# Optimization experiments

Measured on AMD Instinct MI355X. Metric: run time of the kernel, lower is better.

The kernel has to match this reference:

```python
import jax, jax.numpy as jnp
import numpy as np

# graph sizes
G, P, EP = 128, 256, 1024          # graphs, nodes/graph, edges/graph
N, E = G * P, G * EP
C, KENS, S = 4, 2, 1               # centroids, ensembles, samples
R = S * KENS                       # repeats
F, DE, D, OUT = 64, 16, 128, 10


def setup_inputs() -> dict:
    key = jax.random.key(0)
    ks = jax.random.split(key, 24)
    off = (jnp.arange(G, dtype=jnp.int32) * P)[:, None]
    src = (jax.random.randint(ks[0], (G, EP), 0, P, dtype=jnp.int32) + off).reshape(-1)
    dst = (jax.random.randint(ks[1], (G, EP), 0, P, dtype=jnp.int32) + off).reshape(-1)
    edge_index = jnp.stack([src, dst])            # [2, E], edges stay within graphs
    batch = jnp.repeat(jnp.arange(G, dtype=jnp.int32), P)  # [N]
    rn = lambda k, shp, s: jax.random.normal(k, shp, jnp.float32) * s
    return {
        "x_feat": rn(ks[2], (N, F), 1.0),
        "edge_attr": rn(ks[3], (E, DE), 1.0),
        "W_atom": rn(ks[4], (F, D), 0.1), "b_atom": jnp.zeros((D,), jnp.float32),
        "W_score": rn(ks[5], (D, C * KENS), 0.1),
        "W_edge": rn(ks[6], (DE, D), 0.1),
        "W_b2c": rn(ks[7], (D, D), 0.1),
        "W_bb": rn(ks[8], (D, D), 0.1), "W_bc": rn(ks[9], (D, D), 0.1),
        "W_cb": rn(ks[10], (D, D), 0.1), "W_cc": rn(ks[11], (D, D), 0.1),
        "W_sb": rn(ks[12], (D, D), 0.1), "W_sc": rn(ks[13], (D, D), 0.1),
        "W_inter": rn(ks[14], (D, D), 0.1), "b_inter": jnp.zeros((D,), jnp.float32),
        "W_out": rn(ks[15], (D, OUT), 0.1), "b_out": jnp.zeros((OUT,), jnp.float32),
        "edge_index": edge_index, "batch": batch,
    }


def reference(x_feat, edge_attr, W_atom, b_atom, W_score, W_edge, W_b2c,
              W_bb, W_bc, W_cb, W_cc, W_sb, W_sc, W_inter, b_inter,
              W_out, b_out, edge_index, batch):
    src, dst = edge_index[0], edge_index[1]
    # atom encoder + scorer + softmax sampler (marginals)
    x = x_feat @ W_atom + b_atom                                  # [N,D]
    scores = (x @ W_score).reshape(N, C, KENS)
    marg = jax.nn.softmax(scores, axis=1)                         # over centroids
    nm = jnp.broadcast_to(marg[None], (S, N, C, KENS))            # [S,N,C,KENS]
    nm = jnp.transpose(nm, (0, 3, 2, 1)).reshape(R, C, N)         # [R,C,N]
    em = nm[:, :, src] * nm[:, :, dst]                            # edge_mask [R,C,E]
    # base2centroid: masked MP on base graph + weighted segment-mean pooling
    edge_emb = edge_attr @ W_edge                                 # [E,D]
    h = jax.nn.relu(x @ W_b2c)                                    # [N,D]
    m = h[src] + edge_emb                                         # [E,D]
    agg = jnp.zeros((R, C, N, D), m.dtype).at[:, :, dst].add(em[..., None] * m)
    hm = h[None, None] + agg                                      # [R,C,N,D]
    denom = jnp.zeros((R, C, G), nm.dtype).at[:, :, batch].add(nm)
    num = jnp.zeros((R, C, G, D), hm.dtype).at[:, :, batch].add(nm[..., None] * hm)
    cent_x = jnp.transpose(num / (denom[..., None] + 1e-6), (0, 2, 1, 3))  # [R,G,C,D]
    # intra centroid-pair edge weights: triu pairs + diag, scatter over graphs
    iu, ju = np.triu_indices(C, 1)
    pi = np.concatenate([iu, np.arange(C)])
    pj = np.concatenate([ju, np.arange(C)])
    e2g = batch[src]
    w = jnp.zeros((R, pi.size, G), nm.dtype).at[:, :, e2g].add(
        nm[:, pi][:, :, src] * nm[:, pj][:, :, dst])              # [R,10,G]
    w = w.at[:, -C:, :].multiply(0.5)                             # halve diagonal counts
    wt = jnp.transpose(w, (0, 2, 1))                              # [R,G,10]
    Wcc = jnp.zeros((R, G, C, C), nm.dtype)
    Wcc = Wcc.at[:, :, pi, pj].add(wt).at[:, :, pj, pi].add(wt)   # to_undirected
    dg = jnp.arange(C)
    Wcc = Wcc.at[:, :, dg, dg].multiply(0.5)                      # self loops counted once
    Wcc = Wcc / (jax.lax.stop_gradient(jnp.max(Wcc)) + 1e-9)      # detached-max norm
    # hetero GNN layer: base->base, base->centroid, centroid->centroid, centroid->base
    agg_bb = jnp.zeros((N, D), x.dtype).at[dst].add(x[src] + edge_emb)           # [N,D]
    agg_bc = jnp.transpose(
        jnp.zeros((R, C, G, D), x.dtype).at[:, :, batch].add(nm[..., None] * x[None, None]),
        (0, 2, 1, 3))                                             # [R,G,C,D]
    agg_cc = jnp.einsum('rgij,rgjd->rgid', Wcc, cent_x)
    h_cent = jax.nn.relu(agg_bc @ W_bc + agg_cc @ W_cc + cent_x @ W_sc)          # [R,G,C,D]
    agg_cb = jnp.einsum('rcn,rncd->rnd', nm, h_cent[:, batch])                   # [R,N,D]
    h_base = jax.nn.relu(agg_bb[None] @ W_bb + agg_cb @ W_cb + x[None] @ W_sb)   # [R,N,D]
    # inter-ensemble mean pool, inter head, intra mean graph pool, intra head
    node_emb = jnp.mean(h_base, axis=0) @ W_inter + b_inter                      # [N,D]
    graph_emb = jnp.zeros((G, D), node_emb.dtype).at[batch].add(node_emb) / P    # [G,D]
    return graph_emb @ W_out + b_out                                             # [G,OUT]
```

## Files before the change

kernel.cpp:

```cpp
#include <hip/hip_runtime.h>
#include <hip/hip_bf16.h>

#define Nn 32768
#define Ee 131072
#define Gg 128
#define Dd 128

using bf16 = __hip_bfloat16;
typedef __attribute__((ext_vector_type(8))) short bf16x8;
typedef __attribute__((ext_vector_type(4))) float f32x4;

__device__ __forceinline__ float b2f(bf16 v){ return __bfloat162float(v); }
__device__ __forceinline__ bf16  f2b(float v){ return __float2bfloat16(v); }
__device__ __forceinline__ unsigned short bf16bits(float v){
  union { bf16 b; unsigned short u; } cv; cv.b = f2b(v); return cv.u;
}
__device__ __forceinline__ float bfu(unsigned short u){
  return __uint_as_float((unsigned int)u << 16);
}
__device__ __forceinline__ float upk_x(unsigned int v){ return __uint_as_float(v << 16); }
__device__ __forceinline__ float upk_h(unsigned int v){ return __uint_as_float(v & 0xffff0000u); }

__global__ __launch_bounds__(128)
void k_wrep(const float* __restrict__ Wbb, const float* __restrict__ Wsb,
            const float* __restrict__ Wcb, const float* __restrict__ Wa,
            const float* __restrict__ Wb2c,
            unsigned short* __restrict__ Wbbp, unsigned short* __restrict__ Wsbp,
            unsigned short* __restrict__ Wcbp, unsigned short* __restrict__ Wap,
            unsigned short* __restrict__ Wb2cp) {
  int mat = blockIdx.x >> 7, n = blockIdx.x & 127, k = threadIdx.x;
  if      (mat == 0) Wbbp [n*128 + k] = bf16bits(Wbb [k*128 + n]);
  else if (mat == 1) Wsbp [n*128 + k] = bf16bits(Wsb [k*128 + n]);
  else if (mat == 2) Wcbp [n*128 + k] = bf16bits(Wcb [k*128 + n]);
  else if (mat == 3) { if (k < 64) Wap[n*64 + k] = bf16bits(Wa[k*128 + n]); }
  else               Wb2cp[n*128 + k] = bf16bits(Wb2c[k*128 + n]);
}

__global__ __launch_bounds__(256)
void k_atom(const float* __restrict__ xf, const unsigned short* __restrict__ Wap,
            const float* __restrict__ ba, const float* __restrict__ Wsc,
            const unsigned short* __restrict__ Wb2cp,
            unsigned int* __restrict__ xh, float* __restrict__ nmt) {
  __shared__ unsigned short sxf[64*72];
  __shared__ unsigned short sxb[64*136];
  __shared__ float ss[64*8];
  __shared__ float sWsc[1024];
  int tid = threadIdx.x, n0 = blockIdx.x*64;
  int lane = tid & 63, wv = tid >> 6;
  int m = lane & 15, quad = lane >> 4;
  int rbase = wv*16;
  #pragma unroll
  for (int k = 0; k < 4; ++k) {
    int pos = (tid + k*256)*4;
    int node = pos >> 6, f = pos & 63;
    float4 v = *reinterpret_cast<const float4*>(xf + (size_t)n0*64 + pos);
    ushort4 o;
    o.x = bf16bits(v.x); o.y = bf16bits(v.y); o.z = bf16bits(v.z); o.w = bf16bits(v.w);
    *reinterpret_cast<ushort4*>(&sxf[node*72 + f]) = o;
  }
  for (int j = tid; j < 1024; j += 256) sWsc[j] = Wsc[j];
  __syncthreads();
  f32x4 cx[8];
  #pragma unroll
  for (int nt = 0; nt < 8; ++nt) {
    float bv = ba[nt*16 + m];
    cx[nt] = (f32x4){bv, bv, bv, bv};
  }
  const unsigned short* a1 = &sxf[(rbase + m)*72];
  #pragma unroll
  for (int nt = 0; nt < 8; ++nt) {
    #pragma unroll
    for (int kk = 0; kk < 2; ++kk) {
      int ko = kk*32 + quad*8;
      bf16x8 av = *reinterpret_cast<const bf16x8*>((const short*)a1 + ko);
      bf16x8 bv8 = *reinterpret_cast<const bf16x8*>((const short*)Wap + (nt*16 + m)*64 + ko);
      cx[nt] = __builtin_amdgcn_mfma_f32_16x16x32_bf16(av, bv8, cx[nt], 0, 0, 0);
    }
  }
  #pragma unroll
  for (int nt = 0; nt < 8; ++nt)
    #pragma unroll
    for (int i = 0; i < 4; ++i)
      sxb[(rbase + quad*4 + i)*136 + nt*16 + m] = bf16bits(cx[nt][i]);
  __syncthreads();
  for (int p = tid; p < 512; p += 256) {
    int node = p >> 3, col = p & 7;
    float s = 0.f;
    for (int dd = 0; dd < 128; ++dd)
      s += bfu(sxb[node*136 + dd]) * sWsc[dd*8 + col];
    ss[node*8 + col] = s;
  }
  __syncthreads();
  if (tid < 128) {
    int node = tid >> 1, k = tid & 1;
    float v0 = ss[node*8 + 0 + k], v1 = ss[node*8 + 2 + k];
    float v2 = ss[node*8 + 4 + k], v3 = ss[node*8 + 6 + k];
    float mx = fmaxf(fmaxf(v0, v1), fmaxf(v2, v3));
    float e0 = expf(v0-mx), e1 = expf(v1-mx), e2 = expf(v2-mx), e3 = expf(v3-mx);
    float inv = 1.f / (e0+e1+e2+e3);
    *reinterpret_cast<float4*>(nmt + (size_t)(n0 + node)*8 + k*4) =
        make_float4(e0*inv, e1*inv, e2*inv, e3*inv);
  }
  f32x4 chf[8];
  #pragma unroll
  for (int nt = 0; nt < 8; ++nt) chf[nt] = (f32x4){0.f,0.f,0.f,0.f};
  const unsigned short* a2 = &sxb[(rbase + m)*136];
  #pragma unroll
  for (int nt = 0; nt < 8; ++nt) {
    #pragma unroll
    for (int kk = 0; kk < 4; ++kk) {
      int ko = kk*32 + quad*8;
      bf16x8 av = *reinterpret_cast<const bf16x8*>((const short*)a2 + ko);
      bf16x8 bv8 = *reinterpret_cast<const bf16x8*>((const short*)Wb2cp + (nt*16 + m)*128 + ko);
      chf[nt] = __builtin_amdgcn_mfma_f32_16x16x32_bf16(av, bv8, chf[nt], 0, 0, 0);
    }
  }
  #pragma unroll
  for (int nt = 0; nt < 8; ++nt) {
    #pragma unroll
    for (int i = 0; i < 4; ++i) {
      int row = rbase + quad*4 + i, col = nt*16 + m;
      float hv = fmaxf(chf[nt][i], 0.f);
      unsigned short xb = sxb[row*136 + col];
      xh[(size_t)(n0 + row)*128 + col] =
          ((unsigned int)bf16bits(hv) << 16) | (unsigned int)xb;
    }
  }
}

__global__ __launch_bounds__(256)
void k_csr(const int* __restrict__ ei, const float* __restrict__ nmt,
           int* __restrict__ osrc, int* __restrict__ oeid,
           int* __restrict__ rowstart, float* __restrict__ den) {
  __shared__ int cnt[256], off[256], sdl[1024], ssl[1024];
  __shared__ float den8[8];
  int t = threadIdx.x, g = blockIdx.x;
  cnt[t] = 0;
  if (t < 8) den8[t] = 0.f;
  __syncthreads();
  #pragma unroll
  for (int j = 0; j < 4; ++j) {
    int e = t + j*256;
    int sl = ei[g*1024 + e] - g*256;
    int dl = ei[Ee + g*1024 + e] - g*256;
    ssl[e] = sl; sdl[e] = dl;
    atomicAdd(&cnt[dl], 1);
  }
  {
    const float4* p = reinterpret_cast<const float4*>(nmt + (size_t)(g*256 + t)*8);
    float4 a = p[0], b = p[1];
    float v[8] = {a.x,a.y,a.z,a.w,b.x,b.y,b.z,b.w};
    #pragma unroll
    for (int i = 0; i < 8; ++i) {
      float s = v[i];
      for (int o = 32; o > 0; o >>= 1) s += __shfl_xor(s, o);
      if ((t & 63) == 0) atomicAdd(&den8[i], s);
    }
  }
  __syncthreads();
  off[t] = cnt[t];
  __syncthreads();
  for (int s = 1; s < 256; s <<= 1) {
    int v = (t >= s) ? off[t - s] : 0;
    __syncthreads();
    off[t] += v;
    __syncthreads();
  }
  int startv = off[t] - cnt[t];
  rowstart[g*256 + t] = startv;
  off[t] = startv;
  __syncthreads();
  #pragma unroll
  for (int j = 0; j < 4; ++j) {
    int e = t + j*256;
    int pos = atomicAdd(&off[sdl[e]], 1);
    osrc[g*1024 + pos] = g*256 + ssl[e];
    oeid[g*1024 + pos] = e;
  }
  if (t < 8) den[t*Gg + g] = den8[t];
}

__global__ __launch_bounds__(256)
void k_edge(const int* __restrict__ ei, const float* __restrict__ nmt,
            const float* __restrict__ ea, float* __restrict__ bnmp,
            float* __restrict__ geap, float* __restrict__ wsump) {
  __shared__ float eaT[16*260];
  __shared__ float salT[8*260];
  __shared__ float sbeta[8*260];
  __shared__ float red[20];
  __shared__ float sga[256];
  int t = threadIdx.x, bq = blockIdx.x;
  int g = bq >> 2;
  int ebase = g*1024 + (bq & 3)*256;
  for (int j = t; j < 2080; j += 256) sbeta[j] = 0.f;
  if (t < 20) red[t] = 0.f;
  __syncthreads();
  int sl = ei[ebase + t] - g*256;
  int dl = ei[Ee + ebase + t] - g*256;
  const float4* ps4 = reinterpret_cast<const float4*>(nmt + (size_t)(g*256 + sl)*8);
  const float4* pt4 = reinterpret_cast<const float4*>(nmt + (size_t)(g*256 + dl)*8);
  float4 sv0 = ps4[0], sv1 = ps4[1], tv0 = pt4[0], tv1 = pt4[1];
  float ps[8] = {sv0.x,sv0.y,sv0.z,sv0.w,sv1.x,sv1.y,sv1.z,sv1.w};
  float pt[8] = {tv0.x,tv0.y,tv0.z,tv0.w,tv1.x,tv1.y,tv1.z,tv1.w};
  float w20[20];
  #pragma unroll
  for (int r = 0; r < 2; ++r) {
    int b = r*4;
    w20[r*10+0] = ps[b+0]*pt[b+1]; w20[r*10+1] = ps[b+0]*pt[b+2];
    w20[r*10+2] = ps[b+0]*pt[b+3]; w20[r*10+3] = ps[b+1]*pt[b+2];
    w20[r*10+4] = ps[b+1]*pt[b+3]; w20[r*10+5] = ps[b+2]*pt[b+3];
    w20[r*10+6] = ps[b+0]*pt[b+0]; w20[r*10+7] = ps[b+1]*pt[b+1];
    w20[r*10+8] = ps[b+2]*pt[b+2]; w20[r*10+9] = ps[b+3]*pt[b+3];
  }
  #pragma unroll
  for (int rc = 0; rc < 8; ++rc) {
    float al = ps[rc]*pt[rc]*pt[rc];
    salT[rc*260 + t] = al;
    atomicAdd(&sbeta[rc*260 + sl], al);
  }
  {
    const float4* ea4 = reinterpret_cast<const float4*>(ea + (size_t)ebase*16);
    #pragma unroll
    for (int k = 0; k < 4; ++k) {
      float4 v = ea4[t*4 + k];
      eaT[(k*4+0)*260 + t] = v.x;
      eaT[(k*4+1)*260 + t] = v.y;
      eaT[(k*4+2)*260 + t] = v.z;
      eaT[(k*4+3)*260 + t] = v.w;
    }
  }
  #pragma unroll
  for (int i = 0; i < 20; ++i) {
    for (int o = 32; o > 0; o >>= 1) w20[i] += __shfl_down(w20[i], o);
  }
  if ((t & 63) == 0) {
    #pragma unroll
    for (int i = 0; i < 20; ++i) atomicAdd(&red[i], w20[i]);
  }
  __syncthreads();
  {
    int rc = t >> 5, j = (t >> 1) & 15, hf = t & 1;
    float a = 0.f;
    int eb = hf*128;
    for (int ee = eb; ee < eb + 128; ++ee)
      a += salT[rc*260 + ee] * eaT[j*260 + ee];
    sga[t] = a;
  }
  __syncthreads();
  if ((t & 1) == 0) {
    int rc = t >> 5, j = (t >> 1) & 15;
    geap[(size_t)bq*128 + rc*16 + j] = sga[t] + sga[t+1];
  }
  if (t < 20) wsump[bq*20 + t] = red[t];
  {
    float4* bo = reinterpret_cast<float4*>(bnmp + (size_t)bq*2048 + t*8);
    bo[0] = make_float4(sbeta[0*260+t], sbeta[1*260+t], sbeta[2*260+t], sbeta[3*260+t]);
    bo[1] = make_float4(sbeta[4*260+t], sbeta[5*260+t], sbeta[6*260+t], sbeta[7*260+t]);
  }
}

__global__ __launch_bounds__(256)
void k_sea(const float* __restrict__ ea, const int* __restrict__ oeid,
           const int* __restrict__ rowstart, float* __restrict__ sea) {
  int t = threadIdx.x;
  int n = blockIdx.x*16 + (t >> 4);
  int j = t & 15;
  int g = n >> 8;
  int start = rowstart[n];
  int end = ((n & 255) == 255) ? 1024 : rowstart[n+1];
  float s = 0.f;
  for (int jj = start; jj < end; ++jj) {
    int e = oeid[g*1024 + jj];
    s += ea[((size_t)g*1024 + e)*16 + j];
  }
  sea[(size_t)n*16 + j] = s;
}

__global__ __launch_bounds__(128)
void k_wfin(const float* __restrict__ wsump, float* __restrict__ wcc,
            float* __restrict__ maxv) {
  __shared__ float smax[128];
  int t = threadIdx.x;
  float w[20];
  #pragma unroll
  for (int i = 0; i < 20; ++i)
    w[i] = wsump[(t*4+0)*20 + i] + wsump[(t*4+1)*20 + i]
         + wsump[(t*4+2)*20 + i] + wsump[(t*4+3)*20 + i];
  float mx = 0.f;
  #pragma unroll
  for (int r = 0; r < 2; ++r) {
    #pragma unroll
    for (int ij = 0; ij < 16; ++ij) {
      int i = ij >> 2, j = ij & 3;
      float v;
      if (i == j) v = 0.5f * w[r*10 + 6 + i];
      else { int a = i < j ? i : j, b = i < j ? j : i;
             int p = (a == 0) ? (b - 1) : (a == 1) ? (b + 1) : 5;
             v = w[r*10 + p]; }
      wcc[(r*Gg + t)*16 + ij] = v;
      mx = fmaxf(mx, v);
    }
  }
  smax[t] = mx;
  __syncthreads();
  for (int s = 64; s > 0; s >>= 1) {
    if (t < s) smax[t] = fmaxf(smax[t], smax[t + s]);
    __syncthreads();
  }
  if (t == 0) maxv[0] = smax[0];
}

__global__ __launch_bounds__(256)
void k_pool(const unsigned int* __restrict__ xh, const float* __restrict__ nmt,
            const float* __restrict__ bnmp, float* __restrict__ pnum,
            float* __restrict__ pabc) {
  __shared__ float combN[8*128], combA[8*128];
  int t = threadIdx.x, d = t & 127, q = t >> 7;
  int g = blockIdx.x >> 4, e16 = blockIdx.x & 15;
  int nbase = g*256 + e16*16;
  float aH[8] = {0,0,0,0,0,0,0,0};
  float aX[8] = {0,0,0,0,0,0,0,0};
  for (int nn = q; nn < 16; nn += 2) {
    int n = nbase + nn;
    int ln = n & 255;
    unsigned int vn = xh[(size_t)n*128 + d];
    float xn = upk_x(vn), hn = upk_h(vn);
    const float4* pp = reinterpret_cast<const float4*>(nmt + (size_t)n*8);
    float4 p0 = pp[0], p1 = pp[1];
    float pc[8] = {p0.x,p0.y,p0.z,p0.w,p1.x,p1.y,p1.z,p1.w};
    float bt[8] = {0,0,0,0,0,0,0,0};
    #pragma unroll
    for (int qq = 0; qq < 4; ++qq) {
      const float4* bp = reinterpret_cast<const float4*>(bnmp + (size_t)(g*4+qq)*2048 + ln*8);
      float4 b0 = bp[0], b1 = bp[1];
      bt[0]+=b0.x; bt[1]+=b0.y; bt[2]+=b0.z; bt[3]+=b0.w;
      bt[4]+=b1.x; bt[5]+=b1.y; bt[6]+=b1.z; bt[7]+=b1.w;
    }
    #pragma unroll
    for (int rc = 0; rc < 8; ++rc) {
      aH[rc] += (pc[rc] + bt[rc])*hn;
      aX[rc] += pc[rc]*xn;
    }
  }
  if (q == 1) {
    #pragma unroll
    for (int rc = 0; rc < 8; ++rc) { combN[rc*128+d] = aH[rc]; combA[rc*128+d] = aX[rc]; }
  }
  __syncthreads();
  if (q == 0) {
    #pragma unroll
    for (int rc = 0; rc < 8; ++rc) {
      pnum[(((size_t)rc*Gg + g)*16 + e16)*128 + d] = aH[rc] + combN[rc*128+d];
      pabc[(((size_t)rc*Gg + g)*16 + e16)*128 + d] = aX[rc] + combA[rc*128+d];
    }
  }
}

__global__ __launch_bounds__(256)
void k_aggx(const unsigned int* __restrict__ xh, const float* __restrict__ sea,
            const float* __restrict__ We, const int* __restrict__ osrc,
            const int* __restrict__ rowstart, unsigned short* __restrict__ aggbb16) {
  int t = threadIdx.x, d = t & 127, q = t >> 7;
  int g = blockIdx.x >> 5, e32 = blockIdx.x & 31;
  int nbase = g*256 + e32*8;
  float w[16];
  #pragma unroll
  for (int j = 0; j < 16; ++j) w[j] = We[j*128 + d];
  for (int nn = q; nn < 8; nn += 2) {
    int n = nbase + nn;
    const float4* sp = reinterpret_cast<const float4*>(sea + (size_t)n*16);
    float4 s0 = sp[0], s1 = sp[1], s2 = sp[2], s3 = sp[3];
    float agg = s0.x*w[0] + s0.y*w[1] + s0.z*w[2] + s0.w*w[3]
              + s1.x*w[4] + s1.y*w[5] + s1.z*w[6] + s1.w*w[7]
              + s2.x*w[8] + s2.y*w[9] + s2.z*w[10]+ s2.w*w[11]
              + s3.x*w[12]+ s3.y*w[13]+ s3.z*w[14]+ s3.w*w[15];
    int ln = n & 255;
    int start = rowstart[n];
    int end = (ln == 255) ? 1024 : rowstart[n+1];
    for (int jj = start; jj < end; ++jj) {
      int sg = osrc[g*1024 + jj];
      agg += upk_x(xh[(size_t)sg*128 + d]);
    }
    aggbb16[(size_t)n*128 + d] = bf16bits(agg);
  }
}

__global__ __launch_bounds__(128)
void k_hcent(const float* __restrict__ pnum, const float* __restrict__ den,
             const float* __restrict__ pabc, const float* __restrict__ geap,
             const float* __restrict__ We, const float* __restrict__ wcc,
             const float* __restrict__ maxv,
             const float* __restrict__ Wbc, const float* __restrict__ Wcc_,
             const float* __restrict__ Wsc2, float* __restrict__ hcent) {
  __shared__ float scent[512], sbc[512], sccs[512], swcc[16], sgea[64];
  int tid = threadIdx.x, r = blockIdx.x >> 7, g = blockIdx.x & 127;
  float inv = 1.f / (maxv[0] + 1e-9f);
  if (tid < 16) swcc[tid] = wcc[(r*Gg + g)*16 + tid] * inv;
  if (tid < 64) {
    int c = tid >> 4, j = tid & 15;
    int idx = (r*4 + c)*16 + j;
    sgea[tid] = geap[(size_t)(g*4+0)*128 + idx] + geap[(size_t)(g*4+1)*128 + idx]
              + geap[(size_t)(g*4+2)*128 + idx] + geap[(size_t)(g*4+3)*128 + idx];
  }
  __syncthreads();
  for (int c = 0; c < 4; ++c) {
    int rc = r*4 + c;
    float nv = 0.f, av = 0.f;
    #pragma unroll
    for (int s = 0; s < 16; ++s) {
      nv += pnum[(((size_t)rc*Gg + g)*16 + s)*128 + tid];
      av += pabc[(((size_t)rc*Gg + g)*16 + s)*128 + tid];
    }
    #pragma unroll
    for (int j = 0; j < 16; ++j) nv += sgea[c*16 + j] * We[j*128 + tid];
    float dn = den[rc*Gg + g] + 1e-6f;
    scent[c*128 + tid] = nv / dn;
    sbc[c*128 + tid]   = av;
  }
  __syncthreads();
  for (int i = 0; i < 4; ++i) {
    sccs[i*128 + tid] = swcc[i*4+0]*scent[tid]       + swcc[i*4+1]*scent[128 + tid]
                      + swcc[i*4+2]*scent[256 + tid] + swcc[i*4+3]*scent[384 + tid];
  }
  __syncthreads();
  float acc[4] = {0.f, 0.f, 0.f, 0.f};
  for (int k = 0; k < 128; ++k) {
    float wb = Wbc[k*128 + tid], wc = Wcc_[k*128 + tid], ws2 = Wsc2[k*128 + tid];
    #pragma unroll
    for (int c = 0; c < 4; ++c)
      acc[c] += sbc[c*128 + k]*wb + sccs[c*128 + k]*wc + scent[c*128 + k]*ws2;
  }
  #pragma unroll
  for (int c = 0; c < 4; ++c)
    hcent[((r*Gg + g)*4 + c)*128 + tid] = fmaxf(acc[c], 0.f);
}

__global__ __launch_bounds__(256)
void k_hbase(const unsigned short* __restrict__ aggbb16,
             const unsigned int* __restrict__ xh,
             const float* __restrict__ nmt, const float* __restrict__ hcent,
             const unsigned short* __restrict__ Wbbp,
             const unsigned short* __restrict__ Wsbp,
             const unsigned short* __restrict__ Wcbp,
             float* __restrict__ pgsum) {
  __shared__ unsigned short A1[64*136];
  __shared__ unsigned short A2[64*136];
  __shared__ float shc[512];
  __shared__ float snm[256];
  __shared__ float pred[128];
  int tid = threadIdx.x, n0 = blockIdx.x*64, g = n0 >> 8;
  int lane = tid & 63, wv = tid >> 6;
  int m = lane & 15, quad = lane >> 4;
  int rbase = wv*16;
  for (int j = tid; j < 1024; j += 256) {
    int row = j >> 4, col = (j & 15) * 8;
    uint4 v = *reinterpret_cast<const uint4*>(aggbb16 + (size_t)(n0+row)*128 + col);
    *reinterpret_cast<uint4*>(&A1[row*136 + col]) = v;
  }
  for (int j = tid; j < 2048; j += 256) {
    int row = j >> 5, col = (j & 31) * 4;
    uint4 v = *reinterpret_cast<const uint4*>(xh + (size_t)(n0+row)*128 + col);
    uint2 o;
    o.x = (v.x & 0xffffu) | (v.y << 16);
    o.y = (v.z & 0xffffu) | (v.w << 16);
    *reinterpret_cast<uint2*>(&A2[row*136 + col]) = o;
  }
  __syncthreads();
  f32x4 bb[8];
  #pragma unroll
  for (int nt = 0; nt < 8; ++nt) bb[nt] = (f32x4){0.f,0.f,0.f,0.f};
  const short* a1r = (const short*)&A1[(rbase + m)*136];
  const short* a2r = (const short*)&A2[(rbase + m)*136];
  #pragma unroll
  for (int nt = 0; nt < 8; ++nt) {
    #pragma unroll
    for (int kk = 0; kk < 4; ++kk) {
      int ko = kk*32 + quad*8;
      bf16x8 av1 = *reinterpret_cast<const bf16x8*>(a1r + ko);
      bf16x8 wv1 = *reinterpret_cast<const bf16x8*>((const short*)Wbbp + (nt*16 + m)*128 + ko);
      bb[nt] = __builtin_amdgcn_mfma_f32_16x16x32_bf16(av1, wv1, bb[nt], 0, 0, 0);
      bf16x8 av2 = *reinterpret_cast<const bf16x8*>(a2r + ko);
      bf16x8 wv2 = *reinterpret_cast<const bf16x8*>((const short*)Wsbp + (nt*16 + m)*128 + ko);
      bb[nt] = __builtin_amdgcn_mfma_f32_16x16x32_bf16(av2, wv2, bb[nt], 0, 0, 0);
    }
  }
  __syncthreads();
  unsigned short* SB = A2;
  f32x4 msum[8];
  #pragma unroll
  for (int nt = 0; nt < 8; ++nt) msum[nt] = (f32x4){0.f,0.f,0.f,0.f};
  for (int r = 0; r < 2; ++r) {
    for (int j = tid; j < 512; j += 256) shc[j] = hcent[((size_t)(r*Gg + g)*4)*128 + j];
    if (tid < 256) snm[tid] = nmt[(size_t)(n0 + (tid >> 2))*8 + r*4 + (tid & 3)];
    __syncthreads();
    for (int j = tid; j < 8192; j += 256) {
      int node = j >> 7, k = j & 127;
      float v = snm[node*4+0]*shc[k]       + snm[node*4+1]*shc[128 + k]
              + snm[node*4+2]*shc[256 + k] + snm[node*4+3]*shc[384 + k];
      SB[node*136 + k] = bf16bits(v);
    }
    __syncthreads();
    f32x4 aw[8];
    #pragma unroll
    for (int nt = 0; nt < 8; ++nt) aw[nt] = (f32x4){0.f,0.f,0.f,0.f};
    const short* sbr = (const short*)&SB[(rbase + m)*136];
    #pragma unroll
    for (int nt = 0; nt < 8; ++nt) {
      #pragma unroll
      for (int kk = 0; kk < 4; ++kk) {
        int ko = kk*32 + quad*8;
        bf16x8 av = *reinterpret_cast<const bf16x8*>(sbr + ko);
        bf16x8 wvv = *reinterpret_cast<const bf16x8*>((const short*)Wcbp + (nt*16 + m)*128 + ko);
        aw[nt] = __builtin_amdgcn_mfma_f32_16x16x32_bf16(av, wvv, aw[nt], 0, 0, 0);
      }
    }
    #pragma unroll
    for (int nt = 0; nt < 8; ++nt) {
      #pragma unroll
      for (int i = 0; i < 4; ++i)
        msum[nt][i] += 0.5f * fmaxf(bb[nt][i] + aw[nt][i], 0.f);
    }
    __syncthreads();
  }
  if (tid < 128) pred[tid] = 0.f;
  __syncthreads();
  #pragma unroll
  for (int nt = 0; nt < 8; ++nt) {
    float s = msum[nt][0] + msum[nt][1] + msum[nt][2] + msum[nt][3];
    atomicAdd(&pred[nt*16 + m], s);
  }
  __syncthreads();
  if (tid < 128) pgsum[(size_t)blockIdx.x*128 + tid] = pred[tid];
}

__global__ __launch_bounds__(128)
void k_out(const float* __restrict__ pgsum, const float* __restrict__ Wint,
           const float* __restrict__ bint, const float* __restrict__ Wout,
           const float* __restrict__ bout, float* __restrict__ out) {
  __shared__ float ss[128], sge[128];
  int tid = threadIdx.x, g = blockIdx.x;
  float s = pgsum[(size_t)(g*4+0)*128 + tid] + pgsum[(size_t)(g*4+1)*128 + tid]
          + pgsum[(size_t)(g*4+2)*128 + tid] + pgsum[(size_t)(g*4+3)*128 + tid];
  ss[tid] = s * (1.f/256.f);
  __syncthreads();
  float ge = bint[tid];
  for (int k = 0; k < 128; ++k) ge += ss[k] * Wint[k*128 + tid];
  sge[tid] = ge;
  __syncthreads();
  if (tid < 10) {
    float o = bout[tid];
    for (int d = 0; d < 128; ++d) o += sge[d] * Wout[d*10 + tid];
    out[g*10 + tid] = o;
  }
}

extern "C" void kernel_launch(void* const* d_in, const int* in_sizes, int n_in,
                              void* d_out, int out_size, void* d_ws, size_t ws_size,
                              hipStream_t stream) {
  const float* xf   = (const float*)d_in[0];
  const float* ea   = (const float*)d_in[1];
  const float* Wa   = (const float*)d_in[2];
  const float* ba   = (const float*)d_in[3];
  const float* Wsc  = (const float*)d_in[4];
  const float* We   = (const float*)d_in[5];
  const float* Wb2c = (const float*)d_in[6];
  const float* Wbb  = (const float*)d_in[7];
  const float* Wbc  = (const float*)d_in[8];
  const float* Wcb  = (const float*)d_in[9];
  const float* WccW = (const float*)d_in[10];
  const float* Wsb  = (const float*)d_in[11];
  const float* Wsc2 = (const float*)d_in[12];
  const float* Wint = (const float*)d_in[13];
  const float* bint = (const float*)d_in[14];
  const float* Wout = (const float*)d_in[15];
  const float* bout = (const float*)d_in[16];
  const int*   ei   = (const int*)d_in[17];

  float* ws    = (float*)d_ws;
  unsigned int* xh = (unsigned int*)ws;
  float* nmt   = ws + 4194304;
  float* hcent = ws + 4456448;
  float* wcc   = ws + 4587520;
  unsigned short* aggbb16 = (unsigned short*)(ws + 4591616);
  int*   osrc  = (int*)(ws + 6688768);
  int*   oeid  = (int*)(ws + 6819840);
  int*   rowst = (int*)(ws + 6950912);
  float* sea   = ws + 6983680;
  float* bnmp  = ws + 7507968;
  float* geap  = ws + 8556544;
  float* wsump = ws + 8622080;
  float* pnum  = ws + 8632320;
  float* pabc  = ws + 10729472;
  float* den   = ws + 12826624;
  float* pgsum = ws + 12827648;
  float* maxv  = ws + 12893184;
  unsigned short* Wbbp  = (unsigned short*)(ws + 12893248);
  unsigned short* Wsbp  = (unsigned short*)(ws + 12901440);
  unsigned short* Wcbp  = (unsigned short*)(ws + 12909632);
  unsigned short* Wap   = (unsigned short*)(ws + 12917824);
  unsigned short* Wb2cp = (unsigned short*)(ws + 12921920);

  k_wrep <<<5*128, 128, 0, stream>>>(Wbb, Wsb, Wcb, Wa, Wb2c,
                                     Wbbp, Wsbp, Wcbp, Wap, Wb2cp);
  k_atom <<<Nn/64, 256, 0, stream>>>(xf, Wap, ba, Wsc, Wb2cp, xh, nmt);
  k_csr  <<<Gg,    256, 0, stream>>>(ei, nmt, osrc, oeid, rowst, den);
  k_edge <<<Gg*4,  256, 0, stream>>>(ei, nmt, ea, bnmp, geap, wsump);
  k_sea  <<<Nn/16, 256, 0, stream>>>(ea, oeid, rowst, sea);
  k_wfin <<<1,     128, 0, stream>>>(wsump, wcc, maxv);
  k_pool <<<Gg*16, 256, 0, stream>>>(xh, nmt, bnmp, pnum, pabc);
  k_aggx <<<Gg*32, 256, 0, stream>>>(xh, sea, We, osrc, rowst, aggbb16);
  k_hcent<<<2*Gg,  128, 0, stream>>>(pnum, den, pabc, geap, We, wcc, maxv,
                                     Wbc, WccW, Wsc2, hcent);
  k_hbase<<<Nn/64, 256, 0, stream>>>(aggbb16, xh, nmt, hcent, Wbbp, Wsbp, Wcbp, pgsum);
  k_out  <<<Gg,    128, 0, stream>>>(pgsum, Wint, bint, Wout, bout, (float*)d_out);
}
```

Baseline: 281.2 us.

## Merge CSR, edge, and sea kernels; fuse pool with base aggregation

```diff
diff --git a/kernel.cpp b/kernel.cpp
--- a/kernel.cpp
+++ b/kernel.cpp
@@ -129,151 +129,158 @@
 }
 
 __global__ __launch_bounds__(256)
-void k_csr(const int* __restrict__ ei, const float* __restrict__ nmt,
-           int* __restrict__ osrc, int* __restrict__ oeid,
-           int* __restrict__ rowstart, float* __restrict__ den) {
-  __shared__ int cnt[256], off[256], sdl[1024], ssl[1024];
-  __shared__ float den8[8];
-  int t = threadIdx.x, g = blockIdx.x;
-  cnt[t] = 0;
-  if (t < 8) den8[t] = 0.f;
-  __syncthreads();
-  #pragma unroll
-  for (int j = 0; j < 4; ++j) {
-    int e = t + j*256;
-    int sl = ei[g*1024 + e] - g*256;
-    int dl = ei[Ee + g*1024 + e] - g*256;
-    ssl[e] = sl; sdl[e] = dl;
-    atomicAdd(&cnt[dl], 1);
-  }
-  {
-    const float4* p = reinterpret_cast<const float4*>(nmt + (size_t)(g*256 + t)*8);
-    float4 a = p[0], b = p[1];
-    float v[8] = {a.x,a.y,a.z,a.w,b.x,b.y,b.z,b.w};
-    #pragma unroll
-    for (int i = 0; i < 8; ++i) {
-      float s = v[i];
-      for (int o = 32; o > 0; o >>= 1) s += __shfl_xor(s, o);
-      if ((t & 63) == 0) atomicAdd(&den8[i], s);
-    }
-  }
-  __syncthreads();
-  off[t] = cnt[t];
-  __syncthreads();
-  for (int s = 1; s < 256; s <<= 1) {
-    int v = (t >= s) ? off[t - s] : 0;
-    __syncthreads();
-    off[t] += v;
-    __syncthreads();
-  }
-  int startv = off[t] - cnt[t];
-  rowstart[g*256 + t] = startv;
-  off[t] = startv;
-  __syncthreads();
-  #pragma unroll
-  for (int j = 0; j < 4; ++j) {
-    int e = t + j*256;
-    int pos = atomicAdd(&off[sdl[e]], 1);
-    osrc[g*1024 + pos] = g*256 + ssl[e];
-    oeid[g*1024 + pos] = e;
-  }
-  if (t < 8) den[t*Gg + g] = den8[t];
-}
-
-__global__ __launch_bounds__(256)
-void k_edge(const int* __restrict__ ei, const float* __restrict__ nmt,
-            const float* __restrict__ ea, float* __restrict__ bnmp,
-            float* __restrict__ geap, float* __restrict__ wsump) {
-  __shared__ float eaT[16*260];
-  __shared__ float salT[8*260];
-  __shared__ float sbeta[8*260];
-  __shared__ float red[20];
-  __shared__ float sga[256];
-  int t = threadIdx.x, bq = blockIdx.x;
-  int g = bq >> 2;
-  int ebase = g*1024 + (bq & 3)*256;
-  for (int j = t; j < 2080; j += 256) sbeta[j] = 0.f;
-  if (t < 20) red[t] = 0.f;
-  __syncthreads();
-  int sl = ei[ebase + t] - g*256;
-  int dl = ei[Ee + ebase + t] - g*256;
-  const float4* ps4 = reinterpret_cast<const float4*>(nmt + (size_t)(g*256 + sl)*8);
-  const float4* pt4 = reinterpret_cast<const float4*>(nmt + (size_t)(g*256 + dl)*8);
-  float4 sv0 = ps4[0], sv1 = ps4[1], tv0 = pt4[0], tv1 = pt4[1];
-  float ps[8] = {sv0.x,sv0.y,sv0.z,sv0.w,sv1.x,sv1.y,sv1.z,sv1.w};
-  float pt[8] = {tv0.x,tv0.y,tv0.z,tv0.w,tv1.x,tv1.y,tv1.z,tv1.w};
-  float w20[20];
-  #pragma unroll
-  for (int r = 0; r < 2; ++r) {
-    int b = r*4;
-    w20[r*10+0] = ps[b+0]*pt[b+1]; w20[r*10+1] = ps[b+0]*pt[b+2];
-    w20[r*10+2] = ps[b+0]*pt[b+3]; w20[r*10+3] = ps[b+1]*pt[b+2];
-    w20[r*10+4] = ps[b+1]*pt[b+3]; w20[r*10+5] = ps[b+2]*pt[b+3];
-    w20[r*10+6] = ps[b+0]*pt[b+0]; w20[r*10+7] = ps[b+1]*pt[b+1];
-    w20[r*10+8] = ps[b+2]*pt[b+2]; w20[r*10+9] = ps[b+3]*pt[b+3];
-  }
-  #pragma unroll
-  for (int rc = 0; rc < 8; ++rc) {
-    float al = ps[rc]*pt[rc]*pt[rc];
-    salT[rc*260 + t] = al;
-    atomicAdd(&sbeta[rc*260 + sl], al);
-  }
-  {
-    const float4* ea4 = reinterpret_cast<const float4*>(ea + (size_t)ebase*16);
-    #pragma unroll
-    for (int k = 0; k < 4; ++k) {
-      float4 v = ea4[t*4 + k];
-      eaT[(k*4+0)*260 + t] = v.x;
-      eaT[(k*4+1)*260 + t] = v.y;
-      eaT[(k*4+2)*260 + t] = v.z;
-      eaT[(k*4+3)*260 + t] = v.w;
-    }
-  }
-  #pragma unroll
-  for (int i = 0; i < 20; ++i) {
-    for (int o = 32; o > 0; o >>= 1) w20[i] += __shfl_down(w20[i], o);
-  }
-  if ((t & 63) == 0) {
-    #pragma unroll
-    for (int i = 0; i < 20; ++i) atomicAdd(&red[i], w20[i]);
-  }
-  __syncthreads();
-  {
-    int rc = t >> 5, j = (t >> 1) & 15, hf = t & 1;
-    float a = 0.f;
-    int eb = hf*128;
-    for (int ee = eb; ee < eb + 128; ++ee)
-      a += salT[rc*260 + ee] * eaT[j*260 + ee];
-    sga[t] = a;
-  }
-  __syncthreads();
-  if ((t & 1) == 0) {
-    int rc = t >> 5, j = (t >> 1) & 15;
-    geap[(size_t)bq*128 + rc*16 + j] = sga[t] + sga[t+1];
-  }
-  if (t < 20) wsump[bq*20 + t] = red[t];
-  {
-    float4* bo = reinterpret_cast<float4*>(bnmp + (size_t)bq*2048 + t*8);
-    bo[0] = make_float4(sbeta[0*260+t], sbeta[1*260+t], sbeta[2*260+t], sbeta[3*260+t]);
-    bo[1] = make_float4(sbeta[4*260+t], sbeta[5*260+t], sbeta[6*260+t], sbeta[7*260+t]);
-  }
-}
-
-__global__ __launch_bounds__(256)
-void k_sea(const float* __restrict__ ea, const int* __restrict__ oeid,
-           const int* __restrict__ rowstart, float* __restrict__ sea) {
+void k_gedge(const int* __restrict__ ei, const float* __restrict__ nmt,
+             const float* __restrict__ ea,
+             int* __restrict__ osrc, int* __restrict__ rowstart,
+             float* __restrict__ sea, float* __restrict__ den,
+             float* __restrict__ bnmp, float* __restrict__ geap,
+             float* __restrict__ wsump) {
+  __shared__ __align__(16) char smem[34384];
   int t = threadIdx.x;
-  int n = blockIdx.x*16 + (t >> 4);
-  int j = t & 15;
-  int g = n >> 8;
-  int start = rowstart[n];
-  int end = ((n & 255) == 255) ? 1024 : rowstart[n+1];
-  float s = 0.f;
-  for (int jj = start; jj < end; ++jj) {
-    int e = oeid[g*1024 + jj];
-    s += ea[((size_t)g*1024 + e)*16 + j];
-  }
-  sea[(size_t)n*16 + j] = s;
+  if (blockIdx.x < Gg) {
+    int g = blockIdx.x;
+    int* cnt    = (int*)smem;
+    int* off    = cnt + 256;
+    int* sdl    = off + 256;
+    int* ssl    = sdl + 1024;
+    int* sorder = ssl + 1024;
+    float* den8 = (float*)(sorder + 1024);
+    cnt[t] = 0;
+    if (t < 8) den8[t] = 0.f;
+    __syncthreads();
+    #pragma unroll
+    for (int j = 0; j < 4; ++j) {
+      int e = t + j*256;
+      int sl = ei[g*1024 + e] - g*256;
+      int dl = ei[Ee + g*1024 + e] - g*256;
+      ssl[e] = sl; sdl[e] = dl;
+      atomicAdd(&cnt[dl], 1);
+    }
+    {
+      const float4* p = reinterpret_cast<const float4*>(nmt + (size_t)(g*256 + t)*8);
+      float4 a = p[0], b = p[1];
+      float v[8] = {a.x,a.y,a.z,a.w,b.x,b.y,b.z,b.w};
+      #pragma unroll
+      for (int i = 0; i < 8; ++i) {
+        float s = v[i];
+        for (int o = 32; o > 0; o >>= 1) s += __shfl_xor(s, o);
+        if ((t & 63) == 0) atomicAdd(&den8[i], s);
+      }
+    }
+    __syncthreads();
+    off[t] = cnt[t];
+    __syncthreads();
+    for (int s = 1; s < 256; s <<= 1) {
+      int v = (t >= s) ? off[t - s] : 0;
+      __syncthreads();
+      off[t] += v;
+      __syncthreads();
+    }
+    int startv = off[t] - cnt[t];
+    int mycnt = cnt[t];
+    rowstart[g*256 + t] = startv;
+    off[t] = startv;
+    __syncthreads();
+    #pragma unroll
+    for (int j = 0; j < 4; ++j) {
+      int e = t + j*256;
+      int pos = atomicAdd(&off[sdl[e]], 1);
+      osrc[g*1024 + pos] = g*256 + ssl[e];
+      sorder[pos] = e;
+    }
+    __syncthreads();
+    float s0x=0,s0y=0,s0z=0,s0w=0, s1x=0,s1y=0,s1z=0,s1w=0;
+    float s2x=0,s2y=0,s2z=0,s2w=0, s3x=0,s3y=0,s3z=0,s3w=0;
+    for (int jj = startv; jj < startv + mycnt; ++jj) {
+      int e = sorder[jj];
+      const float4* er = reinterpret_cast<const float4*>(ea + ((size_t)g*1024 + e)*16);
+      float4 a0 = er[0], a1 = er[1], a2 = er[2], a3 = er[3];
+      s0x+=a0.x; s0y+=a0.y; s0z+=a0.z; s0w+=a0.w;
+      s1x+=a1.x; s1y+=a1.y; s1z+=a1.z; s1w+=a1.w;
+      s2x+=a2.x; s2y+=a2.y; s2z+=a2.z; s2w+=a2.w;
+      s3x+=a3.x; s3y+=a3.y; s3z+=a3.z; s3w+=a3.w;
+    }
+    float4* so = reinterpret_cast<float4*>(sea + (size_t)(g*256 + t)*16);
+    so[0] = make_float4(s0x,s0y,s0z,s0w);
+    so[1] = make_float4(s1x,s1y,s1z,s1w);
+    so[2] = make_float4(s2x,s2y,s2z,s2w);
+    so[3] = make_float4(s3x,s3y,s3z,s3w);
+    if (t < 8) den[t*Gg + g] = den8[t];
+  } else {
+    int bq = blockIdx.x - Gg;
+    float* eaT   = (float*)smem;
+    float* salT  = eaT + 16*260;
+    float* sbeta = salT + 8*260;
+    float* red   = sbeta + 8*260;
+    float* sga   = red + 20;
+    int g = bq >> 2;
+    int ebase = g*1024 + (bq & 3)*256;
+    for (int j = t; j < 2080; j += 256) sbeta[j] = 0.f;
+    if (t < 20) red[t] = 0.f;
+    __syncthreads();
+    int sl = ei[ebase + t] - g*256;
+    int dl = ei[Ee + ebase + t] - g*256;
+    const float4* ps4 = reinterpret_cast<const float4*>(nmt + (size_t)(g*256 + sl)*8);
+    const float4* pt4 = reinterpret_cast<const float4*>(nmt + (size_t)(g*256 + dl)*8);
+    float4 sv0 = ps4[0], sv1 = ps4[1], tv0 = pt4[0], tv1 = pt4[1];
+    float ps[8] = {sv0.x,sv0.y,sv0.z,sv0.w,sv1.x,sv1.y,sv1.z,sv1.w};
+    float pt[8] = {tv0.x,tv0.y,tv0.z,tv0.w,tv1.x,tv1.y,tv1.z,tv1.w};
+    float w20[20];
+    #pragma unroll
+    for (int r = 0; r < 2; ++r) {
+      int b = r*4;
+      w20[r*10+0] = ps[b+0]*pt[b+1]; w20[r*10+1] = ps[b+0]*pt[b+2];
+      w20[r*10+2] = ps[b+0]*pt[b+3]; w20[r*10+3] = ps[b+1]*pt[b+2];
+      w20[r*10+4] = ps[b+1]*pt[b+3]; w20[r*10+5] = ps[b+2]*pt[b+3];
+      w20[r*10+6] = ps[b+0]*pt[b+0]; w20[r*10+7] = ps[b+1]*pt[b+1];
+      w20[r*10+8] = ps[b+2]*pt[b+2]; w20[r*10+9] = ps[b+3]*pt[b+3];
+    }
+    #pragma unroll
+    for (int rc = 0; rc < 8; ++rc) {
+      float al = ps[rc]*pt[rc]*pt[rc];
+      salT[rc*260 + t] = al;
+      atomicAdd(&sbeta[rc*260 + sl], al);
+    }
+    {
+      const float4* ea4 = reinterpret_cast<const float4*>(ea + (size_t)ebase*16);
+      #pragma unroll
+      for (int k = 0; k < 4; ++k) {
+        float4 v = ea4[t*4 + k];
+        eaT[(k*4+0)*260 + t] = v.x;
+        eaT[(k*4+1)*260 + t] = v.y;
+        eaT[(k*4+2)*260 + t] = v.z;
+        eaT[(k*4+3)*260 + t] = v.w;
+      }
+    }
+    #pragma unroll
+    for (int i = 0; i < 20; ++i) {
+      for (int o = 32; o > 0; o >>= 1) w20[i] += __shfl_down(w20[i], o);
+    }
+    if ((t & 63) == 0) {
+      #pragma unroll
+      for (int i = 0; i < 20; ++i) atomicAdd(&red[i], w20[i]);
+    }
+    __syncthreads();
+    {
+      int rc = t >> 5, j = (t >> 1) & 15, hf = t & 1;
+      float a = 0.f;
+      int eb = hf*128;
+      for (int ee = eb; ee < eb + 128; ++ee)
+        a += salT[rc*260 + ee] * eaT[j*260 + ee];
+      sga[t] = a;
+    }
+    __syncthreads();
+    if ((t & 1) == 0) {
+      int rc = t >> 5, j = (t >> 1) & 15;
+      geap[(size_t)bq*128 + rc*16 + j] = sga[t] + sga[t+1];
+    }
+    if (t < 20) wsump[bq*20 + t] = red[t];
+    {
+      float4* bo = reinterpret_cast<float4*>(bnmp + (size_t)bq*2048 + t*8);
+      bo[0] = make_float4(sbeta[0*260+t], sbeta[1*260+t], sbeta[2*260+t], sbeta[3*260+t]);
+      bo[1] = make_float4(sbeta[4*260+t], sbeta[5*260+t], sbeta[6*260+t], sbeta[7*260+t]);
+    }
+  }
 }
 
 __global__ __launch_bounds__(128)
@@ -311,13 +318,19 @@
 }
 
 __global__ __launch_bounds__(256)
-void k_pool(const unsigned int* __restrict__ xh, const float* __restrict__ nmt,
-            const float* __restrict__ bnmp, float* __restrict__ pnum,
-            float* __restrict__ pabc) {
+void k_poolagg(const unsigned int* __restrict__ xh, const float* __restrict__ nmt,
+               const float* __restrict__ bnmp, const float* __restrict__ sea,
+               const float* __restrict__ We, const int* __restrict__ osrc,
+               const int* __restrict__ rowstart,
+               unsigned short* __restrict__ aggbb16,
+               float* __restrict__ pnum, float* __restrict__ pabc) {
   __shared__ float combN[8*128], combA[8*128];
   int t = threadIdx.x, d = t & 127, q = t >> 7;
   int g = blockIdx.x >> 4, e16 = blockIdx.x & 15;
   int nbase = g*256 + e16*16;
+  float w[16];
+  #pragma unroll
+  for (int j = 0; j < 16; ++j) w[j] = We[j*128 + d];
   float aH[8] = {0,0,0,0,0,0,0,0};
   float aX[8] = {0,0,0,0,0,0,0,0};
   for (int nn = q; nn < 16; nn += 2) {
@@ -341,40 +354,12 @@
       aH[rc] += (pc[rc] + bt[rc])*hn;
       aX[rc] += pc[rc]*xn;
     }
-  }
-  if (q == 1) {
-    #pragma unroll
-    for (int rc = 0; rc < 8; ++rc) { combN[rc*128+d] = aH[rc]; combA[rc*128+d] = aX[rc]; }
-  }
-  __syncthreads();
-  if (q == 0) {
-    #pragma unroll
-    for (int rc = 0; rc < 8; ++rc) {
-      pnum[(((size_t)rc*Gg + g)*16 + e16)*128 + d] = aH[rc] + combN[rc*128+d];
-      pabc[(((size_t)rc*Gg + g)*16 + e16)*128 + d] = aX[rc] + combA[rc*128+d];
-    }
-  }
-}
-
-__global__ __launch_bounds__(256)
-void k_aggx(const unsigned int* __restrict__ xh, const float* __restrict__ sea,
-            const float* __restrict__ We, const int* __restrict__ osrc,
-            const int* __restrict__ rowstart, unsigned short* __restrict__ aggbb16) {
-  int t = threadIdx.x, d = t & 127, q = t >> 7;
-  int g = blockIdx.x >> 5, e32 = blockIdx.x & 31;
-  int nbase = g*256 + e32*8;
-  float w[16];
-  #pragma unroll
-  for (int j = 0; j < 16; ++j) w[j] = We[j*128 + d];
-  for (int nn = q; nn < 8; nn += 2) {
-    int n = nbase + nn;
     const float4* sp = reinterpret_cast<const float4*>(sea + (size_t)n*16);
     float4 s0 = sp[0], s1 = sp[1], s2 = sp[2], s3 = sp[3];
     float agg = s0.x*w[0] + s0.y*w[1] + s0.z*w[2] + s0.w*w[3]
               + s1.x*w[4] + s1.y*w[5] + s1.z*w[6] + s1.w*w[7]
               + s2.x*w[8] + s2.y*w[9] + s2.z*w[10]+ s2.w*w[11]
               + s3.x*w[12]+ s3.y*w[13]+ s3.z*w[14]+ s3.w*w[15];
-    int ln = n & 255;
     int start = rowstart[n];
     int end = (ln == 255) ? 1024 : rowstart[n+1];
     for (int jj = start; jj < end; ++jj) {
@@ -382,6 +367,18 @@
       agg += upk_x(xh[(size_t)sg*128 + d]);
     }
     aggbb16[(size_t)n*128 + d] = bf16bits(agg);
+  }
+  if (q == 1) {
+    #pragma unroll
+    for (int rc = 0; rc < 8; ++rc) { combN[rc*128+d] = aH[rc]; combA[rc*128+d] = aX[rc]; }
+  }
+  __syncthreads();
+  if (q == 0) {
+    #pragma unroll
+    for (int rc = 0; rc < 8; ++rc) {
+      pnum[(((size_t)rc*Gg + g)*16 + e16)*128 + d] = aH[rc] + combN[rc*128+d];
+      pabc[(((size_t)rc*Gg + g)*16 + e16)*128 + d] = aX[rc] + combA[rc*128+d];
+    }
   }
 }
 
@@ -583,7 +580,6 @@
   float* wcc   = ws + 4587520;
   unsigned short* aggbb16 = (unsigned short*)(ws + 4591616);
   int*   osrc  = (int*)(ws + 6688768);
-  int*   oeid  = (int*)(ws + 6819840);
   int*   rowst = (int*)(ws + 6950912);
   float* sea   = ws + 6983680;
   float* bnmp  = ws + 7507968;
@@ -600,17 +596,16 @@
   unsigned short* Wap   = (unsigned short*)(ws + 12917824);
   unsigned short* Wb2cp = (unsigned short*)(ws + 12921920);
 
-  k_wrep <<<5*128, 128, 0, stream>>>(Wbb, Wsb, Wcb, Wa, Wb2c,
-                                     Wbbp, Wsbp, Wcbp, Wap, Wb2cp);
-  k_atom <<<Nn/64, 256, 0, stream>>>(xf, Wap, ba, Wsc, Wb2cp, xh, nmt);
-  k_csr  <<<Gg,    256, 0, stream>>>(ei, nmt, osrc, oeid, rowst, den);
-  k_edge <<<Gg*4,  256, 0, stream>>>(ei, nmt, ea, bnmp, geap, wsump);
-  k_sea  <<<Nn/16, 256, 0, stream>>>(ea, oeid, rowst, sea);
-  k_wfin <<<1,     128, 0, stream>>>(wsump, wcc, maxv);
-  k_pool <<<Gg*16, 256, 0, stream>>>(xh, nmt, bnmp, pnum, pabc);
-  k_aggx <<<Gg*32, 256, 0, stream>>>(xh, sea, We, osrc, rowst, aggbb16);
-  k_hcent<<<2*Gg,  128, 0, stream>>>(pnum, den, pabc, geap, We, wcc, maxv,
-                                     Wbc, WccW, Wsc2, hcent);
-  k_hbase<<<Nn/64, 256, 0, stream>>>(aggbb16, xh, nmt, hcent, Wbbp, Wsbp, Wcbp, pgsum);
-  k_out  <<<Gg,    128, 0, stream>>>(pgsum, Wint, bint, Wout, bout, (float*)d_out);
-}
+  k_wrep   <<<5*128,   128, 0, stream>>>(Wbb, Wsb, Wcb, Wa, Wb2c,
+                                         Wbbp, Wsbp, Wcbp, Wap, Wb2cp);
+  k_atom   <<<Nn/64,   256, 0, stream>>>(xf, Wap, ba, Wsc, Wb2cp, xh, nmt);
+  k_gedge  <<<Gg+Gg*4, 256, 0, stream>>>(ei, nmt, ea, osrc, rowst, sea, den,
+                                         bnmp, geap, wsump);
+  k_wfin   <<<1,       128, 0, stream>>>(wsump, wcc, maxv);
+  k_poolagg<<<Gg*16,   256, 0, stream>>>(xh, nmt, bnmp, sea, We, osrc, rowst,
+                                         aggbb16, pnum, pabc);
+  k_hcent  <<<2*Gg,    128, 0, stream>>>(pnum, den, pabc, geap, We, wcc, maxv,
+                                         Wbc, WccW, Wsc2, hcent);
+  k_hbase  <<<Nn/64,   256, 0, stream>>>(aggbb16, xh, nmt, hcent, Wbbp, Wsbp, Wcbp, pgsum);
+  k_out    <<<Gg,      128, 0, stream>>>(pgsum, Wint, bint, Wout, bout, (float*)d_out);
+}
```

After: 276.4 us. About the same (-1.7%).
